# Kernel tuning notes

Measured on AMD Instinct MI355X. Metric: run time of the kernel, lower is better.

Reference implementation:

```python
import jax, jax.numpy as jnp
import numpy as np

TOP_K = 2
BALANCE_W = 0.01


def setup_inputs() -> dict:
    key = jax.random.key(0)
    ks = jax.random.split(key, 9)
    B, T, D, E, H, S = 4, 2048, 1024, 16, 1024, 2

    def w(k, shape):
        return jax.random.normal(k, shape, jnp.float32) * 0.02

    return {
        "x": jax.random.normal(ks[0], (B, T, D), jnp.float32),
        "router_w": w(ks[1], (D, E)),
        "router_bias": jnp.zeros((E,), jnp.float32),
        "Wg": w(ks[2], (E, D, H)),
        "Wu": w(ks[3], (E, D, H)),
        "Wd": w(ks[4], (E, H, D)),
        "sWg": w(ks[5], (D, S * H)),
        "sWu": w(ks[6], (D, S * H)),
        "sWd": w(ks[7], (S * H, D)),
    }


def reference(x, router_w, router_bias, Wg, Wu, Wd, sWg, sWu, sWd):
    B, T, D = x.shape
    E = router_w.shape[1]
    flat = x.reshape(-1, D)                      # [N, D], N = B*T
    N = flat.shape[0]

    # ---- router (fp32, matching x.float() in torch ref) ----
    logits = flat @ router_w                     # [N, E]
    probs = jax.nn.softmax(logits, axis=-1)      # unbiased probs
    _, indices = jax.lax.top_k(logits + router_bias, TOP_K)  # [N, K]
    weights = jnp.take_along_axis(probs, indices, axis=-1)   # [N, K]
    weights = weights / jnp.maximum(weights.sum(-1, keepdims=True), 1e-9)

    # per-(token, expert) combine weight; top-k indices are unique per row
    C = jnp.zeros((N, E), flat.dtype).at[jnp.arange(N)[:, None], indices].add(weights)
    expert_load = jax.nn.one_hot(indices, E, dtype=jnp.float32).sum((0, 1))  # [E]

    # ---- routed SwiGLU experts: scan over experts, masked combine ----
    def body(acc, per_e):
        wg, wu, wd, c = per_e                    # [D,H],[D,H],[H,D],[N]
        h = jax.nn.silu(flat @ wg) * (flat @ wu) # [N, H]
        return acc + (h @ wd) * c[:, None], None

    routed, _ = jax.lax.scan(body, jnp.zeros_like(flat), (Wg, Wu, Wd, C.T))

    # ---- shared expert ----
    shared = (jax.nn.silu(flat @ sWg) * (flat @ sWu)) @ sWd

    out = (routed + shared).reshape(B, T, D)

    # ---- Switch/DeepSeek balance loss (training mode) ----
    expert_fraction = expert_load / (N * TOP_K)
    probability_fraction = probs.mean(0)
    balance = BALANCE_W * E * jnp.sum(expert_fraction * probability_fraction)

    return out, balance, expert_load
```

## Files before the change

kernel.cpp:

```cpp
#include <hip/hip_runtime.h>
#include <stdint.h>

#define N_TOK 8192
#define DDIM  1024
#define NEXP  16
#define HDIM  1024
#define SHDIM 2048
#define TM 128
#define BK 64
#define MT_R 144

#define SH_GU_NT  32
#define SH_GU_WGS 2048
#define RT_GU_NT  16
#define RT_GU_WGS 2304
#define GU_WGS    4352
#define GU_SLOTS  (GU_WGS / 8)
#define TR2_WGS   4608
#define TR2_SLOTS (TR2_WGS / 8)
#define GUF_WGS   (GU_WGS + TR2_WGS)

#define TND 128
#define DN_WGS    2176

#define TR1_WGS   9216
#define ASG_WGS   64
#define T1A_WGS   (TR1_WGS + ASG_WGS)

#define CPAD 16

typedef __bf16 bf16x8 __attribute__((ext_vector_type(8)));
typedef float  f32x4  __attribute__((ext_vector_type(4)));

__device__ __forceinline__ unsigned short f2bf(float f) {
  union { float f; unsigned u; } v; v.f = f;
  unsigned r = v.u + 0x7fffu + ((v.u >> 16) & 1u);
  return (unsigned short)(r >> 16);
}
__device__ __forceinline__ float bf2f(unsigned short u) {
  union { unsigned u; float f; } v; v.u = (unsigned)u << 16; return v.f;
}

__device__ __forceinline__ void gload16(const void* g, void* l) {
  __builtin_amdgcn_global_load_lds(
      (const __attribute__((address_space(1))) void*)g,
      (__attribute__((address_space(3))) void*)l, 16, 0, 0);
}

__device__ __forceinline__ int xcd_swizzle() {
  int nwg = (int)gridDim.x;
  int b = (int)blockIdx.x;
  return (b & 7) * (nwg >> 3) + (b >> 3);
}

__device__ __forceinline__ bool seg_lookup(const int* __restrict__ cnt, int tm,
                                           int& e, int& segStart, int& segCnt) {
  int o = 0; e = 0; segStart = 0; segCnt = 0;
#pragma unroll
  for (int i = 0; i < NEXP; i++) {
    int c = cnt[i * CPAD];
    if (tm >= o) { e = i; segStart = o; segCnt = c; }
    o += (c + 127) & ~127;
  }
  return tm < o;
}


__global__ void k_zero(int* cnt, int* cursor, float* probsum) {
  int t = threadIdx.x;
  if (t < NEXP * CPAD) { cnt[t] = 0; cursor[t] = 0; probsum[t] = 0.f; }
}

__global__ __launch_bounds__(256) void k_router(
    const float* __restrict__ x, const float* __restrict__ rw,
    const float* __restrict__ rb, int* __restrict__ cnt,
    int* __restrict__ tok_idx, float* __restrict__ tok_w,
    float* __restrict__ probsum, unsigned short* __restrict__ Xbf) {
  __shared__ float rwT[NEXP * 1024];
  __shared__ float ps[NEXP];
  const int t = threadIdx.x;
  if (t < NEXP) ps[t] = 0.f;
  {
    int dbase = t >> 2, e0 = (t & 3) * 4;
#pragma unroll
    for (int c = 0; c < 16; c++) {
      int d = dbase + 64 * c;
      float4 v = *(const float4*)(rw + (size_t)d * NEXP + e0);
      rwT[(e0 + 0) * 1024 + d] = v.x;
      rwT[(e0 + 1) * 1024 + d] = v.y;
      rwT[(e0 + 2) * 1024 + d] = v.z;
      rwT[(e0 + 3) * 1024 + d] = v.w;
    }
  }
  __syncthreads();
  const int lane = t & 63, wv = t >> 6;
  const int tok0 = blockIdx.x * 16 + wv * 4;
  float acc[4][NEXP];
#pragma unroll
  for (int tt = 0; tt < 4; tt++)
#pragma unroll
    for (int e = 0; e < NEXP; e++) acc[tt][e] = 0.f;

#pragma unroll
  for (int c = 0; c < 4; c++) {
    int d = lane * 4 + 256 * c;
    float4 xv[4];
#pragma unroll
    for (int tt = 0; tt < 4; tt++) {
      xv[tt] = *(const float4*)(x + (size_t)(tok0 + tt) * DDIM + d);
      ushort4 o;
      o.x = f2bf(xv[tt].x); o.y = f2bf(xv[tt].y);
      o.z = f2bf(xv[tt].z); o.w = f2bf(xv[tt].w);
      *(ushort4*)(Xbf + (size_t)(tok0 + tt) * DDIM + d) = o;
    }
#pragma unroll
    for (int e = 0; e < NEXP; e++) {
      float4 w4 = *(const float4*)(&rwT[e * 1024 + d]);
#pragma unroll
      for (int tt = 0; tt < 4; tt++) {
        acc[tt][e] = fmaf(xv[tt].x, w4.x, acc[tt][e]);
        acc[tt][e] = fmaf(xv[tt].y, w4.y, acc[tt][e]);
        acc[tt][e] = fmaf(xv[tt].z, w4.z, acc[tt][e]);
        acc[tt][e] = fmaf(xv[tt].w, w4.w, acc[tt][e]);
      }
    }
  }
#pragma unroll
  for (int tt = 0; tt < 4; tt++)
#pragma unroll
    for (int e = 0; e < NEXP; e++) {
      float v = acc[tt][e];
#pragma unroll
      for (int o = 32; o; o >>= 1) v += __shfl_xor(v, o);
      acc[tt][e] = v;
    }

#pragma unroll
  for (int tt = 0; tt < 4; tt++) {
    if (lane == tt) {
      int tok = tok0 + tt;
      float mx = acc[tt][0];
#pragma unroll
      for (int e = 1; e < NEXP; e++) mx = fmaxf(mx, acc[tt][e]);
      float p[NEXP]; float s = 0.f;
#pragma unroll
      for (int e = 0; e < NEXP; e++) { p[e] = __expf(acc[tt][e] - mx); s += p[e]; }
      float inv = 1.f / s;
#pragma unroll
      for (int e = 0; e < NEXP; e++) { p[e] *= inv; atomicAdd(&ps[e], p[e]); }
      int i0 = 0; float b0 = acc[tt][0] + rb[0];
#pragma unroll
      for (int e = 1; e < NEXP; e++) { float v = acc[tt][e] + rb[e]; if (v > b0) { b0 = v; i0 = e; } }
      int i1 = -1; float b1 = -3.4e38f;
#pragma unroll
      for (int e = 0; e < NEXP; e++) {
        if (e == i0) continue;
        float v = acc[tt][e] + rb[e]; if (v > b1) { b1 = v; i1 = e; }
      }
      float w0 = 0.f, w1 = 0.f;
#pragma unroll
      for (int e = 0; e < NEXP; e++) { if (e == i0) w0 = p[e]; if (e == i1) w1 = p[e]; }
      float ssum = fmaxf(w0 + w1, 1e-9f);
      w0 /= ssum; w1 /= ssum;
      atomicAdd(&cnt[i0 * CPAD], 1); atomicAdd(&cnt[i1 * CPAD], 1);
      tok_idx[tok * 2]     = i0; tok_idx[tok * 2 + 1] = i1;
      tok_w[tok * 2]       = w0; tok_w[tok * 2 + 1]   = w1;
    }
  }
  __syncthreads();
  if (t < NEXP) atomicAdd(&probsum[t * CPAD], ps[t]);
}


__device__ __forceinline__ void do_transpose64(
    const float* __restrict__ src, unsigned short* __restrict__ dst,
    int R, int C, int tc, int tr, float* tile ) {
  int rx = threadIdx.x >> 4;
  int cx = (threadIdx.x & 15) * 4;
#pragma unroll
  for (int p = 0; p < 4; p++) {
    int r = p * 16 + rx;
    float4 v = *(const float4*)(src + (size_t)(tr + r) * C + tc + cx);
    tile[(cx + 0) * 65 + r] = v.x;
    tile[(cx + 1) * 65 + r] = v.y;
    tile[(cx + 2) * 65 + r] = v.z;
    tile[(cx + 3) * 65 + r] = v.w;
  }
  __syncthreads();
#pragma unroll
  for (int p = 0; p < 4; p++) {
    int c = p * 16 + rx;
    float v0 = tile[c * 65 + cx + 0];
    float v1 = tile[c * 65 + cx + 1];
    float v2 = tile[c * 65 + cx + 2];
    float v3 = tile[c * 65 + cx + 3];
    ushort4 o; o.x = f2bf(v0); o.y = f2bf(v1); o.z = f2bf(v2); o.w = f2bf(v3);
    *(ushort4*)(dst + (size_t)(tc + c) * R + tr + cx) = o;
  }
}

__global__ __launch_bounds__(256) void k_trgu_assign(
    const float* __restrict__ Wg, const float* __restrict__ Wu,
    const float* __restrict__ sWg, const float* __restrict__ sWu,
    unsigned short* __restrict__ WgT, unsigned short* __restrict__ WuT,
    unsigned short* __restrict__ sWgT, unsigned short* __restrict__ sWuT,
    const int* __restrict__ tok_idx, int* __restrict__ cursor,
    const int* __restrict__ cnt, int* __restrict__ row_token,
    int* __restrict__ tok_rows) {
  __shared__ float tile[64 * 65];
  int id = blockIdx.x;
  if (id < 4096) {
    int mat = id >> 8, tl = id & 255;
    do_transpose64(Wg + ((size_t)mat << 20), WgT + ((size_t)mat << 20),
                   1024, 1024, (tl & 15) * 64, (tl >> 4) * 64, tile);
  } else if (id < 8192) {
    int mat = (id - 4096) >> 8, tl = id & 255;
    do_transpose64(Wu + ((size_t)mat << 20), WuT + ((size_t)mat << 20),
                   1024, 1024, (tl & 15) * 64, (tl >> 4) * 64, tile);
  } else if (id < 8704) {
    int tl = id - 8192;
    do_transpose64(sWg, sWgT, 1024, 2048, (tl & 31) * 64, (tl >> 5) * 64, tile);
  } else if (id < TR1_WGS) {
    int tl = id - 8704;
    do_transpose64(sWu, sWuT, 1024, 2048, (tl & 31) * 64, (tl >> 5) * 64, tile);
  } else {
    int i = (id - TR1_WGS) * 256 + threadIdx.x;
    int e = tok_idx[i];
    int o = 0, myoff = 0;
#pragma unroll
    for (int k = 0; k < NEXP; k++) {
      if (e == k) myoff = o;
      o += (cnt[k * CPAD] + 127) & ~127;
    }
    int pos = atomicAdd(&cursor[e * CPAD], 1);
    int row = myoff + pos;
    row_token[row] = i >> 1;
    tok_rows[i] = row;
  }
}


__global__ __launch_bounds__(256, 4) void k_gateup_all(
    const unsigned short* __restrict__ Xbf,
    const unsigned short* __restrict__ sWgT,
    const unsigned short* __restrict__ sWuT,
    const unsigned short* __restrict__ WgT,
    const unsigned short* __restrict__ WuT,
    unsigned short* __restrict__ Hs,
    unsigned short* __restrict__ Hr,
    const int* __restrict__ cnt,
    const int* __restrict__ row_token,
    const float* __restrict__ Wd, const float* __restrict__ sWd,
    unsigned short* __restrict__ WdT, unsigned short* __restrict__ sWdT) {
  __shared__ __attribute__((aligned(16))) char smem[32768];
  unsigned short* As  = (unsigned short*)smem;
  unsigned short* Bgs = (unsigned short*)(smem + 16384);
  unsigned short* Bus = (unsigned short*)(smem + 24576);

  const int slot = blockIdx.x >> 3;
  const int xcd  = blockIdx.x & 7;

  if (slot >= GU_SLOTS) {
    int tid = xcd * TR2_SLOTS + (slot - GU_SLOTS);
    float* tile = (float*)smem;
    if (tid < 4096) {
      int mat = tid >> 8, tl = tid & 255;
      do_transpose64(Wd + ((size_t)mat << 20), WdT + ((size_t)mat << 20),
                     1024, 1024, (tl & 15) * 64, (tl >> 4) * 64, tile);
    } else {
      int tl = tid - 4096;
      do_transpose64(sWd, sWdT, 2048, 1024, (tl & 15) * 64, (tl >> 4) * 64, tile);
    }
    return;
  }

  const int wg = xcd * GU_SLOTS + slot;
  const int t = threadIdx.x;
  const int lane = t & 63, wv = t >> 6;
  const int lr  = lane >> 3;
  const int kbx = (lane & 7) ^ lr;

  int tm, tn, validEnd, Nh;
  const unsigned short *Bgp, *Bup;
  unsigned short* Hout;
  const unsigned short* pA[4];

  if (wg < SH_GU_WGS) {
    int band = wg >> 9;
    int r = wg & 511;
    tm = (r >> 3) * TM;
    tn = (band * 8 + (r & 7)) * 64;
    validEnd = 0x7fffffff;
    Bgp = sWgT; Bup = sWuT;
    Hout = Hs; Nh = SHDIM;
#pragma unroll
    for (int j = 0; j < 4; j++)
      pA[j] = Xbf + (size_t)(tm + (wv * 4 + j) * 8 + lr) * DDIM;
  } else {
    int u = wg - SH_GU_WGS;
    int band = u / 1152;
    int r = u % 1152;
    tm = (r >> 3) * TM;
    tn = (band * 8 + (r & 7)) * 64;
    int e, segStart, segCnt;
    if (!seg_lookup(cnt, tm, e, segStart, segCnt)) return;
    validEnd = segStart + segCnt;
    Bgp = WgT + (size_t)e * HDIM * DDIM;
    Bup = WuT + (size_t)e * HDIM * DDIM;
    Hout = Hr; Nh = HDIM;
#pragma unroll
    for (int j = 0; j < 4; j++) {
      int row = tm + (wv * 4 + j) * 8 + lr;
      int tok = row < validEnd ? row_token[row] : 0;
      pA[j] = Xbf + (size_t)tok * DDIM;
    }
  }
  const unsigned short* pBg[2];
  const unsigned short* pBu[2];
#pragma unroll
  for (int j = 0; j < 2; j++) {
    int row = tn + (wv * 2 + j) * 8 + lr;
    pBg[j] = Bgp + (size_t)row * DDIM;
    pBu[j] = Bup + (size_t)row * DDIM;
  }

  auto stage = [&](int k0) {
#pragma unroll
    for (int j = 0; j < 4; j++)
      gload16(pA[j] + k0 + kbx * 8, (void*)&As[(wv * 4 + j) * 512]);
#pragma unroll
    for (int j = 0; j < 2; j++) {
      gload16(pBg[j] + k0 + kbx * 8, (void*)&Bgs[(wv * 2 + j) * 512]);
      gload16(pBu[j] + k0 + kbx * 8, (void*)&Bus[(wv * 2 + j) * 512]);
    }
  };

  f32x4 accG[4][2] = {};
  f32x4 accU[4][2] = {};
  const int wr = wv >> 1, wc = wv & 1;
  const int rbase = lane & 15;
  const int kgrp = lane >> 4;

  for (int k0 = 0; k0 < DDIM; k0 += BK) {
    if (k0) __syncthreads();
    stage(k0);
    __syncthreads();
#pragma unroll
    for (int kk = 0; kk < 2; kk++) {
      bf16x8 af[4], gf[2], uf[2];
      int kbl = kk * 4 + kgrp;
#pragma unroll
      for (int i = 0; i < 4; i++) {
        int r = wr * 64 + i * 16 + rbase;
        af[i] = *(const bf16x8*)((const char*)As + r * 128 + ((kbl ^ (r & 7)) << 4));
      }
#pragma unroll
      for (int j = 0; j < 2; j++) {
        int r = wc * 32 + j * 16 + rbase;
        gf[j] = *(const bf16x8*)((const char*)Bgs + r * 128 + ((kbl ^ (r & 7)) << 4));
        uf[j] = *(const bf16x8*)((const char*)Bus + r * 128 + ((kbl ^ (r & 7)) << 4));
      }
#pragma unroll
      for (int i = 0; i < 4; i++)
#pragma unroll
        for (int j = 0; j < 2; j++) {
          accG[i][j] = __builtin_amdgcn_mfma_f32_16x16x32_bf16(af[i], gf[j], accG[i][j], 0, 0, 0);
          accU[i][j] = __builtin_amdgcn_mfma_f32_16x16x32_bf16(af[i], uf[j], accU[i][j], 0, 0, 0);
        }
    }
  }

  const int orow0 = tm + wr * 64 + (lane >> 4) * 4;
  const int ocol0 = tn + wc * 32 + (lane & 15);
#pragma unroll
  for (int i = 0; i < 4; i++)
#pragma unroll
    for (int j = 0; j < 2; j++)
#pragma unroll
      for (int r = 0; r < 4; r++) {
        int row = orow0 + i * 16 + r;
        if (row < validEnd) {
          float g = accG[i][j][r], u = accU[i][j][r];
          float h = g / (1.f + __expf(-g)) * u;
          Hout[(size_t)row * Nh + ocol0 + j * 16] = f2bf(h);
        }
      }
}

__global__ __launch_bounds__(256, 4) void k_down_all(
    const unsigned short* __restrict__ Hs,
    const unsigned short* __restrict__ Hr,
    const unsigned short* __restrict__ sWdT,
    const unsigned short* __restrict__ WdT,
    float* __restrict__ out,
    float* __restrict__ Pbuf,
    unsigned short* __restrict__ Rbuf,
    const int* __restrict__ cnt) {
  __shared__ unsigned short As[TM * BK];
  __shared__ unsigned short Bs[TND * BK];

  const int wg = xcd_swizzle();
  const int t = threadIdx.x;
  const int lane = t & 63, wv = t >> 6;
  const int lr  = lane >> 3;
  const int kbx = (lane & 7) ^ lr;

  int tm, tn, validEnd;
  bool routed;
  float* outF = out;
  const unsigned short* pA[4];
  const unsigned short* pB[4];

  if (wg < 1024) {
    routed = false;
    int half = wg >> 9;
    int r = wg & 511;
    tm = (r >> 3) * TM;
    tn = (r & 7) * TND;
    validEnd = 0x7fffffff;
    outF = half ? Pbuf : out;
    int kbase = half << 10;
#pragma unroll
    for (int j = 0; j < 4; j++) {
      pA[j] = Hs + (size_t)(tm + (wv * 4 + j) * 8 + lr) * SHDIM + kbase;
      pB[j] = sWdT + (size_t)(tn + (wv * 4 + j) * 8 + lr) * SHDIM + kbase;
    }
  } else {
    routed = true;
    int wgr = wg - 1024;
    tm = (wgr >> 3) * TM;
    tn = (wgr & 7) * TND;
    int e, segStart, segCnt;
    if (!seg_lookup(cnt, tm, e, segStart, segCnt)) return;
    validEnd = segStart + segCnt;
    const unsigned short* B = WdT + (size_t)e * DDIM * HDIM;
#pragma unroll
    for (int j = 0; j < 4; j++) {
      pA[j] = Hr + (size_t)(tm + (wv * 4 + j) * 8 + lr) * HDIM;
      pB[j] = B + (size_t)(tn + (wv * 4 + j) * 8 + lr) * HDIM;
    }
  }

  auto stage = [&](int k0) {
#pragma unroll
    for (int j = 0; j < 4; j++) {
      gload16(pA[j] + k0 + kbx * 8, (void*)&As[(wv * 4 + j) * 512]);
      gload16(pB[j] + k0 + kbx * 8, (void*)&Bs[(wv * 4 + j) * 512]);
    }
  };

  f32x4 acc[4][4] = {};
  const int wr = wv >> 1, wc = wv & 1;
  const int rbase = lane & 15;
  const int kgrp = lane >> 4;

  for (int k0 = 0; k0 < 1024; k0 += BK) {
    if (k0) __syncthreads();
    stage(k0);
    __syncthreads();
#pragma unroll
    for (int kk = 0; kk < 2; kk++) {
      bf16x8 af[4], bf[4];
      int kbl = kk * 4 + kgrp;
#pragma unroll
      for (int i = 0; i < 4; i++) {
        int r = wr * 64 + i * 16 + rbase;
        af[i] = *(const bf16x8*)((const char*)&As[0] + r * 128 + ((kbl ^ (r & 7)) << 4));
      }
#pragma unroll
      for (int j = 0; j < 4; j++) {
        int r = wc * 64 + j * 16 + rbase;
        bf[j] = *(const bf16x8*)((const char*)&Bs[0] + r * 128 + ((kbl ^ (r & 7)) << 4));
      }
#pragma unroll
      for (int i = 0; i < 4; i++)
#pragma unroll
        for (int j = 0; j < 4; j++)
          acc[i][j] = __builtin_amdgcn_mfma_f32_16x16x32_bf16(af[i], bf[j], acc[i][j], 0, 0, 0);
    }
  }

  const int orow0 = tm + wr * 64 + (lane >> 4) * 4;
  const int ocol0 = tn + wc * 64 + (lane & 15);
#pragma unroll
  for (int i = 0; i < 4; i++)
#pragma unroll
    for (int j = 0; j < 4; j++)
#pragma unroll
      for (int r = 0; r < 4; r++) {
        int row = orow0 + i * 16 + r;
        int col = ocol0 + j * 16;
        if (routed) {
          if (row < validEnd) Rbuf[(size_t)row * DDIM + col] = f2bf(acc[i][j][r]);
        } else {
          outF[(size_t)row * DDIM + col] = acc[i][j][r];
        }
      }
}

__global__ __launch_bounds__(256) void k_combine(
    float* __restrict__ out, const float* __restrict__ Pbuf,
    const unsigned short* __restrict__ Rbuf,
    const int* __restrict__ tok_rows, const float* __restrict__ tok_w,
    const float* __restrict__ probsum, const int* __restrict__ cnt,
    float* __restrict__ out_tail) {
  int tok = blockIdx.x;
  int c = threadIdx.x;
  int r0 = tok_rows[tok * 2], r1 = tok_rows[tok * 2 + 1];
  float w0 = tok_w[tok * 2],  w1 = tok_w[tok * 2 + 1];
  float4 o  = ((const float4*)(out + (size_t)tok * DDIM))[c];
  float4 p  = ((const float4*)(Pbuf + (size_t)tok * DDIM))[c];
  ushort4 a = ((const ushort4*)(Rbuf + (size_t)r0 * DDIM))[c];
  ushort4 b = ((const ushort4*)(Rbuf + (size_t)r1 * DDIM))[c];
  o.x += p.x + w0 * bf2f(a.x) + w1 * bf2f(b.x);
  o.y += p.y + w0 * bf2f(a.y) + w1 * bf2f(b.y);
  o.z += p.z + w0 * bf2f(a.z) + w1 * bf2f(b.z);
  o.w += p.w + w0 * bf2f(a.w) + w1 * bf2f(b.w);
  ((float4*)(out + (size_t)tok * DDIM))[c] = o;

  if (blockIdx.x == 0) {
    if (threadIdx.x == 0) {
      float bal = 0.f;
      for (int e = 0; e < NEXP; e++) {
        float frac = (float)cnt[e * CPAD] / (float)(N_TOK * 2);
        bal += frac * (probsum[e * CPAD] / (float)N_TOK);
      }
      out_tail[0] = 0.01f * (float)NEXP * bal;
    }
    if (threadIdx.x < NEXP) out_tail[1 + threadIdx.x] = (float)cnt[threadIdx.x * CPAD];
  }
}


extern "C" void kernel_launch(void* const* d_in, const int* in_sizes, int n_in,
                              void* d_out, int out_size, void* d_ws, size_t ws_size,
                              hipStream_t stream) {
  const float* x   = (const float*)d_in[0];
  const float* rw  = (const float*)d_in[1];
  const float* rb  = (const float*)d_in[2];
  const float* Wg  = (const float*)d_in[3];
  const float* Wu  = (const float*)d_in[4];
  const float* Wd  = (const float*)d_in[5];
  const float* sWg = (const float*)d_in[6];
  const float* sWu = (const float*)d_in[7];
  const float* sWd = (const float*)d_in[8];
  float* out = (float*)d_out;

  uint8_t* w = (uint8_t*)d_ws;
  size_t off = 0;
  auto alloc = [&](size_t bytes) -> void* {
    void* p = w + off;
    off += (bytes + 255) & ~(size_t)255;
    return p;
  };

  int*   cnt      = (int*)alloc(NEXP * CPAD * 4);
  int*   cursor   = (int*)alloc(NEXP * CPAD * 4);
  float* probsum  = (float*)alloc(NEXP * CPAD * 4);
  int*   tok_idx  = (int*)alloc((size_t)N_TOK * 2 * 4);
  float* tok_w    = (float*)alloc((size_t)N_TOK * 2 * 4);
  int*   tok_rows = (int*)alloc((size_t)N_TOK * 2 * 4);
  int*   row_tok  = (int*)alloc((size_t)MT_R * TM * 4);
  unsigned short* Xbf  = (unsigned short*)alloc((size_t)N_TOK * DDIM * 2);
  unsigned short* Hs   = (unsigned short*)alloc((size_t)N_TOK * SHDIM * 2);
  unsigned short* Hr   = (unsigned short*)alloc((size_t)MT_R * TM * HDIM * 2);
  unsigned short* Rbuf = (unsigned short*)alloc((size_t)MT_R * TM * DDIM * 2);
  unsigned short* WgT  = (unsigned short*)alloc((size_t)NEXP * HDIM * DDIM * 2);
  unsigned short* WuT  = (unsigned short*)alloc((size_t)NEXP * HDIM * DDIM * 2);
  unsigned short* WdT  = (unsigned short*)alloc((size_t)NEXP * DDIM * HDIM * 2);
  unsigned short* sWgT = (unsigned short*)alloc((size_t)SHDIM * DDIM * 2);
  unsigned short* sWuT = (unsigned short*)alloc((size_t)SHDIM * DDIM * 2);
  unsigned short* sWdT = (unsigned short*)alloc((size_t)DDIM * SHDIM * 2);

  float* Pbuf = (float*)WgT;

  if (off > ws_size) return;

  k_zero<<<1, 256, 0, stream>>>(cnt, cursor, probsum);
  k_router<<<N_TOK / 16, 256, 0, stream>>>(x, rw, rb, cnt, tok_idx, tok_w, probsum, Xbf);
  k_trgu_assign<<<T1A_WGS, 256, 0, stream>>>(
      Wg, Wu, sWg, sWu, WgT, WuT, sWgT, sWuT,
      tok_idx, cursor, cnt, row_tok, tok_rows);
  k_gateup_all<<<GUF_WGS, 256, 0, stream>>>(
      Xbf, sWgT, sWuT, WgT, WuT, Hs, Hr, cnt, row_tok,
      Wd, sWd, WdT, sWdT);
  k_down_all<<<DN_WGS, 256, 0, stream>>>(
      Hs, Hr, sWdT, WdT, out, Pbuf, Rbuf, cnt);
  k_combine<<<N_TOK, 256, 0, stream>>>(
      out, Pbuf, Rbuf, tok_rows, tok_w, probsum, cnt, out + (size_t)N_TOK * DDIM);
}
```

Before: 390.3 us.

## Fuse router with gate/up weight transposes; split token assignment into own kernel

New measurement: 395.4 us. No clear change (+1.3%).

```diff
diff --git a/kernel.cpp b/kernel.cpp
--- a/kernel.cpp
+++ b/kernel.cpp
@@ -23,9 +23,9 @@
 #define TND 128
 #define DN_WGS    2176
 
+#define RT_WGS    512
 #define TR1_WGS   9216
-#define ASG_WGS   64
-#define T1A_WGS   (TR1_WGS + ASG_WGS)
+#define RTF_WGS   (RT_WGS + TR1_WGS)
 
 #define CPAD 16
 
@@ -63,112 +63,6 @@
     o += (c + 127) & ~127;
   }
   return tm < o;
-}
-
-
-__global__ void k_zero(int* cnt, int* cursor, float* probsum) {
-  int t = threadIdx.x;
-  if (t < NEXP * CPAD) { cnt[t] = 0; cursor[t] = 0; probsum[t] = 0.f; }
-}
-
-__global__ __launch_bounds__(256) void k_router(
-    const float* __restrict__ x, const float* __restrict__ rw,
-    const float* __restrict__ rb, int* __restrict__ cnt,
-    int* __restrict__ tok_idx, float* __restrict__ tok_w,
-    float* __restrict__ probsum, unsigned short* __restrict__ Xbf) {
-  __shared__ float rwT[NEXP * 1024];
-  __shared__ float ps[NEXP];
-  const int t = threadIdx.x;
-  if (t < NEXP) ps[t] = 0.f;
-  {
-    int dbase = t >> 2, e0 = (t & 3) * 4;
-#pragma unroll
-    for (int c = 0; c < 16; c++) {
-      int d = dbase + 64 * c;
-      float4 v = *(const float4*)(rw + (size_t)d * NEXP + e0);
-      rwT[(e0 + 0) * 1024 + d] = v.x;
-      rwT[(e0 + 1) * 1024 + d] = v.y;
-      rwT[(e0 + 2) * 1024 + d] = v.z;
-      rwT[(e0 + 3) * 1024 + d] = v.w;
-    }
-  }
-  __syncthreads();
-  const int lane = t & 63, wv = t >> 6;
-  const int tok0 = blockIdx.x * 16 + wv * 4;
-  float acc[4][NEXP];
-#pragma unroll
-  for (int tt = 0; tt < 4; tt++)
-#pragma unroll
-    for (int e = 0; e < NEXP; e++) acc[tt][e] = 0.f;
-
-#pragma unroll
-  for (int c = 0; c < 4; c++) {
-    int d = lane * 4 + 256 * c;
-    float4 xv[4];
-#pragma unroll
-    for (int tt = 0; tt < 4; tt++) {
-      xv[tt] = *(const float4*)(x + (size_t)(tok0 + tt) * DDIM + d);
-      ushort4 o;
-      o.x = f2bf(xv[tt].x); o.y = f2bf(xv[tt].y);
-      o.z = f2bf(xv[tt].z); o.w = f2bf(xv[tt].w);
-      *(ushort4*)(Xbf + (size_t)(tok0 + tt) * DDIM + d) = o;
-    }
-#pragma unroll
-    for (int e = 0; e < NEXP; e++) {
-      float4 w4 = *(const float4*)(&rwT[e * 1024 + d]);
-#pragma unroll
-      for (int tt = 0; tt < 4; tt++) {
-        acc[tt][e] = fmaf(xv[tt].x, w4.x, acc[tt][e]);
-        acc[tt][e] = fmaf(xv[tt].y, w4.y, acc[tt][e]);
-        acc[tt][e] = fmaf(xv[tt].z, w4.z, acc[tt][e]);
-        acc[tt][e] = fmaf(xv[tt].w, w4.w, acc[tt][e]);
-      }
-    }
-  }
-#pragma unroll
-  for (int tt = 0; tt < 4; tt++)
-#pragma unroll
-    for (int e = 0; e < NEXP; e++) {
-      float v = acc[tt][e];
-#pragma unroll
-      for (int o = 32; o; o >>= 1) v += __shfl_xor(v, o);
-      acc[tt][e] = v;
-    }
-
-#pragma unroll
-  for (int tt = 0; tt < 4; tt++) {
-    if (lane == tt) {
-      int tok = tok0 + tt;
-      float mx = acc[tt][0];
-#pragma unroll
-      for (int e = 1; e < NEXP; e++) mx = fmaxf(mx, acc[tt][e]);
-      float p[NEXP]; float s = 0.f;
-#pragma unroll
-      for (int e = 0; e < NEXP; e++) { p[e] = __expf(acc[tt][e] - mx); s += p[e]; }
-      float inv = 1.f / s;
-#pragma unroll
-      for (int e = 0; e < NEXP; e++) { p[e] *= inv; atomicAdd(&ps[e], p[e]); }
-      int i0 = 0; float b0 = acc[tt][0] + rb[0];
-#pragma unroll
-      for (int e = 1; e < NEXP; e++) { float v = acc[tt][e] + rb[e]; if (v > b0) { b0 = v; i0 = e; } }
-      int i1 = -1; float b1 = -3.4e38f;
-#pragma unroll
-      for (int e = 0; e < NEXP; e++) {
-        if (e == i0) continue;
-        float v = acc[tt][e] + rb[e]; if (v > b1) { b1 = v; i1 = e; }
-      }
-      float w0 = 0.f, w1 = 0.f;
-#pragma unroll
-      for (int e = 0; e < NEXP; e++) { if (e == i0) w0 = p[e]; if (e == i1) w1 = p[e]; }
-      float ssum = fmaxf(w0 + w1, 1e-9f);
-      w0 /= ssum; w1 /= ssum;
-      atomicAdd(&cnt[i0 * CPAD], 1); atomicAdd(&cnt[i1 * CPAD], 1);
-      tok_idx[tok * 2]     = i0; tok_idx[tok * 2 + 1] = i1;
-      tok_w[tok * 2]       = w0; tok_w[tok * 2 + 1]   = w1;
-    }
-  }
-  __syncthreads();
-  if (t < NEXP) atomicAdd(&probsum[t * CPAD], ps[t]);
 }
 
 
@@ -199,44 +93,155 @@
   }
 }
 
-__global__ __launch_bounds__(256) void k_trgu_assign(
+
+__global__ void k_zero(int* cnt, int* cursor, float* probsum) {
+  int t = threadIdx.x;
+  if (t < NEXP * CPAD) { cnt[t] = 0; cursor[t] = 0; probsum[t] = 0.f; }
+}
+
+__global__ __launch_bounds__(256) void k_router_tr(
+    const float* __restrict__ x, const float* __restrict__ rw,
+    const float* __restrict__ rb, int* __restrict__ cnt,
+    int* __restrict__ tok_idx, float* __restrict__ tok_w,
+    float* __restrict__ probsum, unsigned short* __restrict__ Xbf,
     const float* __restrict__ Wg, const float* __restrict__ Wu,
     const float* __restrict__ sWg, const float* __restrict__ sWu,
     unsigned short* __restrict__ WgT, unsigned short* __restrict__ WuT,
-    unsigned short* __restrict__ sWgT, unsigned short* __restrict__ sWuT,
+    unsigned short* __restrict__ sWgT, unsigned short* __restrict__ sWuT) {
+  __shared__ __attribute__((aligned(16))) float smem[NEXP * 1024 + NEXP];
+  const int t = threadIdx.x;
+
+  if (blockIdx.x >= RT_WGS) {
+    int id = blockIdx.x - RT_WGS;
+    float* tile = smem;
+    if (id < 4096) {
+      int mat = id >> 8, tl = id & 255;
+      do_transpose64(Wg + ((size_t)mat << 20), WgT + ((size_t)mat << 20),
+                     1024, 1024, (tl & 15) * 64, (tl >> 4) * 64, tile);
+    } else if (id < 8192) {
+      int mat = (id - 4096) >> 8, tl = id & 255;
+      do_transpose64(Wu + ((size_t)mat << 20), WuT + ((size_t)mat << 20),
+                     1024, 1024, (tl & 15) * 64, (tl >> 4) * 64, tile);
+    } else if (id < 8704) {
+      int tl = id - 8192;
+      do_transpose64(sWg, sWgT, 1024, 2048, (tl & 31) * 64, (tl >> 5) * 64, tile);
+    } else {
+      int tl = id - 8704;
+      do_transpose64(sWu, sWuT, 1024, 2048, (tl & 31) * 64, (tl >> 5) * 64, tile);
+    }
+    return;
+  }
+
+  float* rwT = smem;
+  float* ps  = smem + NEXP * 1024;
+  if (t < NEXP) ps[t] = 0.f;
+  {
+    int dbase = t >> 2, e0 = (t & 3) * 4;
+#pragma unroll
+    for (int c = 0; c < 16; c++) {
+      int d = dbase + 64 * c;
+      float4 v = *(const float4*)(rw + (size_t)d * NEXP + e0);
+      rwT[(e0 + 0) * 1024 + d] = v.x;
+      rwT[(e0 + 1) * 1024 + d] = v.y;
+      rwT[(e0 + 2) * 1024 + d] = v.z;
+      rwT[(e0 + 3) * 1024 + d] = v.w;
+    }
+  }
+  __syncthreads();
+  const int lane = t & 63, wv = t >> 6;
+  const int tok0 = blockIdx.x * 16 + wv * 4;
+  float acc[4][NEXP];
+#pragma unroll
+  for (int tt = 0; tt < 4; tt++)
+#pragma unroll
+    for (int e = 0; e < NEXP; e++) acc[tt][e] = 0.f;
+
+#pragma unroll
+  for (int c = 0; c < 4; c++) {
+    int d = lane * 4 + 256 * c;
+    float4 xv[4];
+#pragma unroll
+    for (int tt = 0; tt < 4; tt++) {
+      xv[tt] = *(const float4*)(x + (size_t)(tok0 + tt) * DDIM + d);
+      ushort4 o;
+      o.x = f2bf(xv[tt].x); o.y = f2bf(xv[tt].y);
+      o.z = f2bf(xv[tt].z); o.w = f2bf(xv[tt].w);
+      *(ushort4*)(Xbf + (size_t)(tok0 + tt) * DDIM + d) = o;
+    }
+#pragma unroll
+    for (int e = 0; e < NEXP; e++) {
+      float4 w4 = *(const float4*)(&rwT[e * 1024 + d]);
+#pragma unroll
+      for (int tt = 0; tt < 4; tt++) {
+        acc[tt][e] = fmaf(xv[tt].x, w4.x, acc[tt][e]);
+        acc[tt][e] = fmaf(xv[tt].y, w4.y, acc[tt][e]);
+        acc[tt][e] = fmaf(xv[tt].z, w4.z, acc[tt][e]);
+        acc[tt][e] = fmaf(xv[tt].w, w4.w, acc[tt][e]);
+      }
+    }
+  }
+#pragma unroll
+  for (int tt = 0; tt < 4; tt++)
+#pragma unroll
+    for (int e = 0; e < NEXP; e++) {
+      float v = acc[tt][e];
+#pragma unroll
+      for (int o = 32; o; o >>= 1) v += __shfl_xor(v, o);
+      acc[tt][e] = v;
+    }
+
+#pragma unroll
+  for (int tt = 0; tt < 4; tt++) {
+    if (lane == tt) {
+      int tok = tok0 + tt;
+      float mx = acc[tt][0];
+#pragma unroll
+      for (int e = 1; e < NEXP; e++) mx = fmaxf(mx, acc[tt][e]);
+      float p[NEXP]; float s = 0.f;
+#pragma unroll
+      for (int e = 0; e < NEXP; e++) { p[e] = __expf(acc[tt][e] - mx); s += p[e]; }
+      float inv = 1.f / s;
+#pragma unroll
+      for (int e = 0; e < NEXP; e++) { p[e] *= inv; atomicAdd(&ps[e], p[e]); }
+      int i0 = 0; float b0 = acc[tt][0] + rb[0];
+#pragma unroll
+      for (int e = 1; e < NEXP; e++) { float v = acc[tt][e] + rb[e]; if (v > b0) { b0 = v; i0 = e; } }
+      int i1 = -1; float b1 = -3.4e38f;
+#pragma unroll
+      for (int e = 0; e < NEXP; e++) {
+        if (e == i0) continue;
+        float v = acc[tt][e] + rb[e]; if (v > b1) { b1 = v; i1 = e; }
+      }
+      float w0 = 0.f, w1 = 0.f;
+#pragma unroll
+      for (int e = 0; e < NEXP; e++) { if (e == i0) w0 = p[e]; if (e == i1) w1 = p[e]; }
+      float ssum = fmaxf(w0 + w1, 1e-9f);
+      w0 /= ssum; w1 /= ssum;
+      atomicAdd(&cnt[i0 * CPAD], 1); atomicAdd(&cnt[i1 * CPAD], 1);
+      tok_idx[tok * 2]     = i0; tok_idx[tok * 2 + 1] = i1;
+      tok_w[tok * 2]       = w0; tok_w[tok * 2 + 1]   = w1;
+    }
+  }
+  __syncthreads();
+  if (t < NEXP) atomicAdd(&probsum[t * CPAD], ps[t]);
+}
+
+__global__ __launch_bounds__(256) void k_assign(
     const int* __restrict__ tok_idx, int* __restrict__ cursor,
     const int* __restrict__ cnt, int* __restrict__ row_token,
     int* __restrict__ tok_rows) {
-  __shared__ float tile[64 * 65];
-  int id = blockIdx.x;
-  if (id < 4096) {
-    int mat = id >> 8, tl = id & 255;
-    do_transpose64(Wg + ((size_t)mat << 20), WgT + ((size_t)mat << 20),
-                   1024, 1024, (tl & 15) * 64, (tl >> 4) * 64, tile);
-  } else if (id < 8192) {
-    int mat = (id - 4096) >> 8, tl = id & 255;
-    do_transpose64(Wu + ((size_t)mat << 20), WuT + ((size_t)mat << 20),
-                   1024, 1024, (tl & 15) * 64, (tl >> 4) * 64, tile);
-  } else if (id < 8704) {
-    int tl = id - 8192;
-    do_transpose64(sWg, sWgT, 1024, 2048, (tl & 31) * 64, (tl >> 5) * 64, tile);
-  } else if (id < TR1_WGS) {
-    int tl = id - 8704;
-    do_transpose64(sWu, sWuT, 1024, 2048, (tl & 31) * 64, (tl >> 5) * 64, tile);
-  } else {
-    int i = (id - TR1_WGS) * 256 + threadIdx.x;
-    int e = tok_idx[i];
-    int o = 0, myoff = 0;
-#pragma unroll
-    for (int k = 0; k < NEXP; k++) {
-      if (e == k) myoff = o;
-      o += (cnt[k * CPAD] + 127) & ~127;
-    }
-    int pos = atomicAdd(&cursor[e * CPAD], 1);
-    int row = myoff + pos;
-    row_token[row] = i >> 1;
-    tok_rows[i] = row;
-  }
+  int i = blockIdx.x * 256 + threadIdx.x;
+  int e = tok_idx[i];
+  int o = 0, myoff = 0;
+#pragma unroll
+  for (int k = 0; k < NEXP; k++) {
+    if (e == k) myoff = o;
+    o += (cnt[k * CPAD] + 127) & ~127;
+  }
+  int pos = atomicAdd(&cursor[e * CPAD], 1);
+  int row = myoff + pos;
+  row_token[row] = i >> 1;
+  tok_rows[i] = row;
 }
 
 
@@ -305,6 +310,7 @@
     int e, segStart, segCnt;
     if (!seg_lookup(cnt, tm, e, segStart, segCnt)) return;
     validEnd = segStart + segCnt;
+    if (tm >= validEnd) return;
     Bgp = WgT + (size_t)e * HDIM * DDIM;
     Bup = WuT + (size_t)e * HDIM * DDIM;
     Hout = Hr; Nh = HDIM;
@@ -433,6 +439,7 @@
     int e, segStart, segCnt;
     if (!seg_lookup(cnt, tm, e, segStart, segCnt)) return;
     validEnd = segStart + segCnt;
+    if (tm >= validEnd) return;
     const unsigned short* B = WdT + (size_t)e * DDIM * HDIM;
 #pragma unroll
     for (int j = 0; j < 4; j++) {
@@ -577,10 +584,10 @@
   if (off > ws_size) return;
 
   k_zero<<<1, 256, 0, stream>>>(cnt, cursor, probsum);
-  k_router<<<N_TOK / 16, 256, 0, stream>>>(x, rw, rb, cnt, tok_idx, tok_w, probsum, Xbf);
-  k_trgu_assign<<<T1A_WGS, 256, 0, stream>>>(
-      Wg, Wu, sWg, sWu, WgT, WuT, sWgT, sWuT,
-      tok_idx, cursor, cnt, row_tok, tok_rows);
+  k_router_tr<<<RTF_WGS, 256, 0, stream>>>(
+      x, rw, rb, cnt, tok_idx, tok_w, probsum, Xbf,
+      Wg, Wu, sWg, sWu, WgT, WuT, sWgT, sWuT);
+  k_assign<<<64, 256, 0, stream>>>(tok_idx, cursor, cnt, row_tok, tok_rows);
   k_gateup_all<<<GUF_WGS, 256, 0, stream>>>(
       Xbf, sWgT, sWuT, WgT, WuT, Hs, Hr, cnt, row_tok,
       Wd, sWd, WdT, sWdT);
```
